# Performance work log

Measured on AMD Instinct MI355X. Metric: run time of the kernel, lower is better.

The kernel has to match this reference:

```python
import jax, jax.numpy as jnp
import numpy as np
import math

B, LQ, C = 4, 2048, 256
NH, NL, NP = 8, 4, 8
HD = C // NH
SHAPES = [(128, 128), (64, 64), (32, 32), (16, 16)]


def _grid_init_bias():
    thetas = np.arange(NH, dtype=np.float32) * (2.0 * math.pi / NH)
    g = np.stack([np.cos(thetas), np.sin(thetas)], -1)
    g = g / np.abs(g).max(-1, keepdims=True)
    g = np.tile(g[:, None, None, :], (1, NL, NP, 1))
    g = g * ((np.arange(NP, dtype=np.float32) + 1.0) / NP)[None, None, :, None]
    return jnp.asarray(g.reshape(-1), jnp.float32)


def setup_inputs() -> dict:
    key = jax.random.key(0)
    ks = jax.random.split(key, 12)
    Lv = sum(h * w for h, w in SHAPES)
    query = jax.random.normal(ks[0], (B, LQ, C), jnp.float32)
    reference_points = jax.random.uniform(ks[1], (B, LQ, NL, 2), jnp.float32)
    value = jax.random.normal(ks[2], (B, Lv, C), jnp.float32)
    spatial_shapes = jnp.asarray(np.array(SHAPES, np.int32))
    starts = np.cumsum([0] + [h * w for h, w in SHAPES])[:-1]
    level_start_index = jnp.asarray(starts.astype(np.int32))
    OFF = NH * NL * NP * 2
    return {
        'query': query,
        'reference_points': reference_points,
        'value': value,
        'spatial_shapes': spatial_shapes,
        'level_start_index': level_start_index,
        'W_off': jax.random.normal(ks[3], (C, OFF), jnp.float32) * 0.01,
        'b_off': _grid_init_bias(),
        'W_attn': jax.random.normal(ks[4], (C, NH * NL * NP), jnp.float32) * 0.01,
        'b_attn': jnp.zeros((NH * NL * NP,), jnp.float32),
        'Wa1': jax.random.normal(ks[5], (C, C // 2), jnp.float32) * 0.02,
        'ba1': jnp.zeros((C // 2,), jnp.float32),
        'Wa2': jax.random.normal(ks[6], (C // 2, OFF), jnp.float32) * 0.02,
        'ba2': jnp.zeros((OFF,), jnp.float32),
        'Wv': jax.random.normal(ks[7], (C, C), jnp.float32) * (1.0 / math.sqrt(C)),
        'bv': jnp.zeros((C,), jnp.float32),
        'Wo': jax.random.normal(ks[8], (C, C), jnp.float32) * (1.0 / math.sqrt(C)),
        'bo': jnp.zeros((C,), jnp.float32),
    }


def _bilinear(vflat, gx, gy, H, W):
    # vflat: [B, nh, H*W, hd]; gx, gy: [B, Lq, nh, P] in grid coords [-1, 1]
    # Matches F.grid_sample(mode='bilinear', padding_mode='zeros', align_corners=False)
    Bq, Lq, nh, P = gx.shape
    hd = vflat.shape[-1]
    x = ((gx + 1.0) * W - 1.0) * 0.5
    y = ((gy + 1.0) * H - 1.0) * 0.5
    x0f = jnp.floor(x); y0f = jnp.floor(y)
    lx = x - x0f; ly = y - y0f
    x0 = x0f.astype(jnp.int32); y0 = y0f.astype(jnp.int32)
    out = jnp.zeros((Bq, Lq, nh, P, hd), vflat.dtype)
    corners = ((0, 0, (1 - lx) * (1 - ly)), (1, 0, lx * (1 - ly)),
               (0, 1, (1 - lx) * ly), (1, 1, lx * ly))
    for dx, dy, w in corners:
        xi = x0 + dx; yi = y0 + dy
        valid = (xi >= 0) & (xi < W) & (yi >= 0) & (yi < H)
        idx = jnp.clip(yi, 0, H - 1) * W + jnp.clip(xi, 0, W - 1)
        idx_t = idx.transpose(0, 2, 1, 3).reshape(Bq, nh, Lq * P)
        g = jnp.take_along_axis(vflat, idx_t[..., None], axis=2)  # [B, nh, Lq*P, hd]
        g = g.reshape(Bq, nh, Lq, P, hd).transpose(0, 2, 1, 3, 4)
        out = out + g * (w * valid.astype(vflat.dtype))[..., None]
    return out


def reference(query, reference_points, value, spatial_shapes, level_start_index,
              W_off, b_off, W_attn, b_attn, Wa1, ba1, Wa2, ba2, Wv, bv, Wo, bo):
    shapes = np.asarray(spatial_shapes)
    starts = np.asarray(level_start_index)
    Bq, Lq, _ = query.shape

    v = (value @ Wv + bv).reshape(Bq, -1, NH, HD)            # [B, Lv, nh, hd]
    off = (query @ W_off + b_off).reshape(Bq, Lq, NH, NL, NP, 2)
    hid = jax.nn.relu(query @ Wa1 + ba1)
    off = off + 0.1 * (hid @ Wa2 + ba2).reshape(Bq, Lq, NH, NL, NP, 2)
    aw = jax.nn.softmax((query @ W_attn + b_attn).reshape(Bq, Lq, NH, NL * NP), -1)
    aw = aw.reshape(Bq, Lq, NH, NL, NP)

    # offset normalizer is (W, H) per level
    norm = jnp.stack([spatial_shapes[:, 1], spatial_shapes[:, 0]], -1).astype(query.dtype)
    loc = reference_points[:, :, None, :, None, :] + off / norm[None, None, None, :, None, :]
    grid = loc * 2.0 - 1.0                                    # [B, Lq, nh, NL, NP, 2]

    acc = jnp.zeros((Bq, Lq, NH, HD), query.dtype)
    for lvl in range(NL):
        H, W = int(shapes[lvl, 0]), int(shapes[lvl, 1])
        s = int(starts[lvl]); e = s + H * W
        vl = v[:, s:e].transpose(0, 2, 1, 3)                  # [B, nh, H*W, hd]
        gx = grid[:, :, :, lvl, :, 0]
        gy = grid[:, :, :, lvl, :, 1]
        samp = _bilinear(vl, gx, gy, H, W)                    # [B, Lq, nh, P, hd]
        acc = acc + jnp.einsum('blhpd,blhp->blhd', samp, aw[:, :, :, lvl, :])
    out = acc.reshape(Bq, Lq, NH * HD)
    return out @ Wo + bo
```

## Files before the change

### kernel.cpp

```cpp
#include <hip/hip_runtime.h>
#include <math.h>

#define B_SZ 4
#define LQ_SZ 2048
#define C_SZ 256
#define NH_SZ 8
#define NL_SZ 4
#define NP_SZ 8
#define HD_SZ 32
#define LV_SZ 21760
#define NQ_SZ (B_SZ * LQ_SZ)
#define MV_SZ (B_SZ * LV_SZ)

typedef __attribute__((ext_vector_type(8))) short bf16x8;
typedef __attribute__((ext_vector_type(8))) unsigned short ushort8;
typedef __attribute__((ext_vector_type(4))) float f32x4;

__device__ __forceinline__ float bf2f(unsigned short u) {
  union { float f; unsigned v; } x;
  x.v = ((unsigned)u) << 16;
  return x.f;
}
__device__ __forceinline__ unsigned short f2bf(float f) {
  union { float f; unsigned v; } x;
  x.f = f;
  unsigned r = x.v + 0x7fffu + ((x.v >> 16) & 1u);
  return (unsigned short)(r >> 16);
}

__device__ __forceinline__ bf16x8 cvt8(f32x4 a, f32x4 b) {
  union { unsigned u[4]; bf16x8 v; } r;
  asm("v_cvt_pk_bf16_f32 %0, %1, %2" : "=v"(r.u[0]) : "v"(a[0]), "v"(a[1]));
  asm("v_cvt_pk_bf16_f32 %0, %1, %2" : "=v"(r.u[1]) : "v"(a[2]), "v"(a[3]));
  asm("v_cvt_pk_bf16_f32 %0, %1, %2" : "=v"(r.u[2]) : "v"(b[0]), "v"(b[1]));
  asm("v_cvt_pk_bf16_f32 %0, %1, %2" : "=v"(r.u[3]) : "v"(b[2]), "v"(b[3]));
  return r.v;
}

__device__ __forceinline__ int swz(int x) {
  return ((x & 1) << 2) | ((x >> 1) & 3);
}

__global__ void prep_weights(
    const float* __restrict__ Wv, const float* __restrict__ Wo,
    const float* __restrict__ W_off, const float* __restrict__ W_attn,
    const float* __restrict__ Wa1, const float* __restrict__ Wa2,
    const float* __restrict__ b_off, const float* __restrict__ b_attn,
    const float* __restrict__ ba1,
    unsigned short* __restrict__ wtv, unsigned short* __restrict__ wto,
    unsigned short* __restrict__ wcat, unsigned short* __restrict__ wa2t,
    float* __restrict__ bcat) {
  const int bid = blockIdx.x, t = threadIdx.x;
  if (bid < 256) {
    wtv[bid * 256 + t] = f2bf(Wv[t * 256 + bid]);
  } else if (bid < 512) {
    const int n = bid - 256;
    wto[n * 256 + t] = f2bf(Wo[t * 256 + n]);
  } else if (bid < 1536) {
    const int n = bid - 512;
    float v;
    if (n < 512) v = W_off[t * 512 + n];
    else if (n < 768) v = W_attn[t * 256 + (n - 512)];
    else if (n < 896) v = Wa1[t * 128 + (n - 768)];
    else v = 0.f;
    wcat[n * 256 + t] = f2bf(v);
  } else if (bid < 1792) {
    const int idx = (bid - 1536) * 256 + t;
    const int n = idx >> 7, k = idx & 127;
    wa2t[n * 128 + k] = f2bf(Wa2[k * 512 + n]);
  } else {
    const int idx = (bid - 1792) * 256 + t;
    float v;
    if (idx < 512) v = b_off[idx];
    else if (idx < 768) v = b_attn[idx - 512];
    else if (idx < 896) v = ba1[idx - 768];
    else v = 0.f;
    bcat[idx] = v;
  }
}

template <int MODE, int A_BF16, int K_DIM>
__global__ __launch_bounds__(512, 2) void gemm_wave(
    const void* __restrict__ Ain, const unsigned short* __restrict__ Wt,
    const float* __restrict__ bias, void* __restrict__ Cout,
    unsigned short* __restrict__ aux, int n_total) {
  constexpr int KSTEPS = K_DIM / 32;
  constexpr int CHUNKS = K_DIM / 8;
  __shared__ unsigned short Bs[128 * K_DIM];
  const int tid = threadIdx.x;
  const int lane = tid & 63;
  const int w = tid >> 6;
  const int rowc = lane & 15, rowg = lane >> 4;
  const int bn0 = blockIdx.x * 128;
  const long bm = (long)blockIdx.y * 128;

  {
    const int row = tid >> 2, qq = tid & 3;
    const unsigned short* src = Wt + (long)(bn0 + row) * K_DIM;
    char* dstrow = (char*)Bs + row * (K_DIM * 2);
    const int sz = swz(row);
#pragma unroll
    for (int i = 0; i < CHUNKS / 4; ++i) {
      const int cl = i * 4 + qq;
      ushort8 u = *(const ushort8*)(src + cl * 8);
      *(ushort8*)(dstrow + (cl ^ sz) * 16) = u;
    }
  }

  bf16x8 afrag[KSTEPS];
  if constexpr (A_BF16) {
    const unsigned short* ap =
        (const unsigned short*)Ain + (bm + w * 16 + rowc) * (long)K_DIM +
        rowg * 8;
#pragma unroll
    for (int ks = 0; ks < KSTEPS; ++ks)
      afrag[ks] = *(const bf16x8*)(ap + ks * 32);
  } else {
    const float* ap =
        (const float*)Ain + (bm + w * 16 + rowc) * (long)K_DIM + rowg * 8;
#pragma unroll
    for (int ks = 0; ks < KSTEPS; ++ks) {
      f32x4 x0 = *(const f32x4*)(ap + ks * 32);
      f32x4 x1 = *(const f32x4*)(ap + ks * 32 + 4);
      afrag[ks] = cvt8(x0, x1);
    }
  }

  f32x4 acc[8];
#pragma unroll
  for (int n = 0; n < 8; ++n) acc[n] = (f32x4){0.f, 0.f, 0.f, 0.f};

  __syncthreads();

#pragma unroll
  for (int ks = 0; ks < KSTEPS; ++ks) {
#pragma unroll
    for (int n = 0; n < 8; ++n) {
      const int col = n * 16 + rowc;
      const int cs = (ks * 4 + rowg) ^ swz(col);
      bf16x8 bf =
          *(const bf16x8*)((const char*)Bs + col * (K_DIM * 2) + cs * 16);
      acc[n] = __builtin_amdgcn_mfma_f32_16x16x32_bf16(bf, afrag[ks], acc[n],
                                                       0, 0, 0);
    }
  }

  const long row = bm + w * 16 + rowc;
#pragma unroll
  for (int n = 0; n < 8; ++n) {
    const int col = bn0 + n * 16 + rowg * 4;
    const float4 bb = *(const float4*)(bias + col);
    const float v0 = acc[n][0] + bb.x;
    const float v1 = acc[n][1] + bb.y;
    const float v2 = acc[n][2] + bb.z;
    const float v3 = acc[n][3] + bb.w;
    if constexpr (MODE == 0) {
      float4 s = {v0, v1, v2, v3};
      *(float4*)((float*)Cout + row * n_total + col) = s;
    } else if constexpr (MODE == 1) {
      union { unsigned u[2]; uint2 d; } pk;
      asm("v_cvt_pk_bf16_f32 %0, %1, %2" : "=v"(pk.u[0]) : "v"(v0), "v"(v1));
      asm("v_cvt_pk_bf16_f32 %0, %1, %2" : "=v"(pk.u[1]) : "v"(v2), "v"(v3));
      *(uint2*)((unsigned short*)Cout + row * n_total + col) = pk.d;
    } else {
      if (bn0 < 768) {
        float4 s = {v0, v1, v2, v3};
        *(float4*)((float*)Cout + row * n_total + col) = s;
      } else {
        union { unsigned u[2]; uint2 d; } pk;
        const float r0 = fmaxf(v0, 0.f), r1 = fmaxf(v1, 0.f);
        const float r2 = fmaxf(v2, 0.f), r3 = fmaxf(v3, 0.f);
        asm("v_cvt_pk_bf16_f32 %0, %1, %2" : "=v"(pk.u[0]) : "v"(r0), "v"(r1));
        asm("v_cvt_pk_bf16_f32 %0, %1, %2" : "=v"(pk.u[1]) : "v"(r2), "v"(r3));
        *(uint2*)(aux + row * 128 + (col - 768)) = pk.d;
      }
    }
  }
}

__global__ __launch_bounds__(256) void sample_kernel(
    const unsigned short* __restrict__ v, const float* __restrict__ proj,
    const float* __restrict__ off2, const float* __restrict__ refpts,
    float* __restrict__ acc_out) {
  __shared__ int4 sidx[512];
  __shared__ float4 sw[512];
  const int tid = threadIdx.x;
  const long q0 = (long)blockIdx.x * 2;
  const int b = (int)(q0 >> 11);
  constexpr int starts[4] = {0, 16384, 20480, 21504};

#pragma unroll
  for (int ss = 0; ss < 2; ++ss) {
    const int s = tid + ss * 256;
    const int qq = s >> 8, j = s & 255;
    const long qi = q0 + qq;
    const int l = (j >> 3) & 3;
    const int HW = 128 >> l;
    const float fHW = (float)HW;

    const float logit = proj[qi * 1024 + 512 + j];
    float mx = logit;
#pragma unroll
    for (int mask = 16; mask > 0; mask >>= 1)
      mx = fmaxf(mx, __shfl_xor(mx, mask));
    const float e = __expf(logit - mx);
    float sum = e;
#pragma unroll
    for (int mask = 16; mask > 0; mask >>= 1) sum += __shfl_xor(sum, mask);
    const float wgt = e / sum;

    const float2 po = *(const float2*)(proj + qi * 1024 + 2 * j);
    const float2 o2 = *(const float2*)(off2 + qi * 512 + 2 * j);
    const float2 rp = *(const float2*)(refpts + qi * 8 + l * 2);
    const float rnorm = 1.f / fHW;
    const float gx = (rp.x + (po.x + 0.1f * o2.x) * rnorm) * 2.f - 1.f;
    const float gy = (rp.y + (po.y + 0.1f * o2.y) * rnorm) * 2.f - 1.f;

    const float x = ((gx + 1.f) * fHW - 1.f) * 0.5f;
    const float y = ((gy + 1.f) * fHW - 1.f) * 0.5f;
    const float x0f = floorf(x), y0f = floorf(y);
    const float lx = x - x0f, ly = y - y0f;
    const int ix0 = (int)x0f, iy0 = (int)y0f;
    const int ix1 = ix0 + 1, iy1 = iy0 + 1;
    const float vx0 = (ix0 >= 0 && ix0 < HW) ? 1.f : 0.f;
    const float vx1 = (ix1 >= 0 && ix1 < HW) ? 1.f : 0.f;
    const float vy0 = (iy0 >= 0 && iy0 < HW) ? 1.f : 0.f;
    const float vy1 = (iy1 >= 0 && iy1 < HW) ? 1.f : 0.f;
    const int cx0 = min(max(ix0, 0), HW - 1);
    const int cx1 = min(max(ix1, 0), HW - 1);
    const int cy0 = min(max(iy0, 0), HW - 1);
    const int cy1 = min(max(iy1, 0), HW - 1);
    const int base = starts[l];
    int4 o;
    o.x = (base + cy0 * HW + cx0) * 512;
    o.y = (base + cy0 * HW + cx1) * 512;
    o.z = (base + cy1 * HW + cx0) * 512;
    o.w = (base + cy1 * HW + cx1) * 512;
    sidx[s] = o;
    float4 wv;
    wv.x = (1.f - lx) * (1.f - ly) * vx0 * vy0 * wgt;
    wv.y = lx * (1.f - ly) * vx1 * vy0 * wgt;
    wv.z = (1.f - lx) * ly * vx0 * vy1 * wgt;
    wv.w = lx * ly * vx1 * vy1 * wgt;
    sw[s] = wv;
  }
  __syncthreads();

  const int qq = tid >> 7, h = (tid >> 4) & 7, dp = tid & 15;
  const char* vb =
      (const char*)v + ((long)b * LV_SZ * 256 + h * 32 + dp * 2) * 2;
  const int sbase = qq * 256 + h * 32;
  float acc0 = 0.f, acc1 = 0.f;
#pragma unroll 8
  for (int j = 0; j < 32; ++j) {
    const int4 o = sidx[sbase + j];
    const float4 w = sw[sbase + j];
    const ushort2 u0 = *(const ushort2*)(vb + o.x);
    const ushort2 u1 = *(const ushort2*)(vb + o.y);
    const ushort2 u2 = *(const ushort2*)(vb + o.z);
    const ushort2 u3 = *(const ushort2*)(vb + o.w);
    acc0 = fmaf(bf2f(u0.x), w.x, acc0);
    acc1 = fmaf(bf2f(u0.y), w.x, acc1);
    acc0 = fmaf(bf2f(u1.x), w.y, acc0);
    acc1 = fmaf(bf2f(u1.y), w.y, acc1);
    acc0 = fmaf(bf2f(u2.x), w.z, acc0);
    acc1 = fmaf(bf2f(u2.y), w.z, acc1);
    acc0 = fmaf(bf2f(u3.x), w.w, acc0);
    acc1 = fmaf(bf2f(u3.y), w.w, acc1);
  }
  float2 res = {acc0, acc1};
  *(float2*)(acc_out + (q0 + qq) * 256 + h * 32 + dp * 2) = res;
}

extern "C" void kernel_launch(void* const* d_in, const int* in_sizes, int n_in,
                              void* d_out, int out_size, void* d_ws,
                              size_t ws_size, hipStream_t stream) {
  const float* query  = (const float*)d_in[0];
  const float* refpts = (const float*)d_in[1];
  const float* value  = (const float*)d_in[2];
  const float* W_off  = (const float*)d_in[5];
  const float* b_off  = (const float*)d_in[6];
  const float* W_attn = (const float*)d_in[7];
  const float* b_attn = (const float*)d_in[8];
  const float* Wa1    = (const float*)d_in[9];
  const float* ba1    = (const float*)d_in[10];
  const float* Wa2    = (const float*)d_in[11];
  const float* ba2    = (const float*)d_in[12];
  const float* Wv     = (const float*)d_in[13];
  const float* bv     = (const float*)d_in[14];
  const float* Wo     = (const float*)d_in[15];
  const float* bo     = (const float*)d_in[16];
  float* out = (float*)d_out;

  char* ws = (char*)d_ws;
  unsigned short* v_ws = (unsigned short*)ws;
  float* proj_ws = (float*)(ws + 44564480);
  float* off2_ws = (float*)(ws + 78118912);
  unsigned short* wcat_ws = (unsigned short*)(ws + 78118912);
  unsigned short* hidb_ws = (unsigned short*)(ws + 94896128);
  float* acc_ws  = (float*)(ws + 96993280);
  unsigned short* wtv_ws  = (unsigned short*)(ws + 122159104);
  unsigned short* wto_ws  = (unsigned short*)(ws + 122290176);
  unsigned short* wa2t_ws = (unsigned short*)(ws + 122421248);
  float* bcat_ws = (float*)(ws + 122552320);

  prep_weights<<<1796, 256, 0, stream>>>(Wv, Wo, W_off, W_attn, Wa1, Wa2,
                                         b_off, b_attn, ba1, wtv_ws, wto_ws,
                                         wcat_ws, wa2t_ws, bcat_ws);
  gemm_wave<1, 0, 256><<<dim3(2, MV_SZ / 128), 512, 0, stream>>>(
      value, wtv_ws, bv, v_ws, nullptr, 256);
  gemm_wave<2, 0, 256><<<dim3(7, NQ_SZ / 128), 512, 0, stream>>>(
      query, wcat_ws, bcat_ws, proj_ws, hidb_ws, 1024);
  gemm_wave<0, 1, 128><<<dim3(4, NQ_SZ / 128), 512, 0, stream>>>(
      hidb_ws, wa2t_ws, ba2, off2_ws, nullptr, 512);
  sample_kernel<<<NQ_SZ / 2, 256, 0, stream>>>(v_ws, proj_ws, off2_ws, refpts,
                                               acc_ws);
  gemm_wave<0, 0, 256><<<dim3(2, NQ_SZ / 128), 512, 0, stream>>>(
      acc_ws, wto_ws, bo, out, nullptr, 256);
}
```

Before: 122.8 us.

## Make value projection GEMM persistent with weight tile reuse and A prefetch

Replaces the 1360-block value-projection GEMM with a 512-block persistent kernel. Each block loads its 128-column bf16 weight slice into LDS once and then loops over row tiles with a stride of 256. While the MFMAs for the current tile run, it prefetches and converts the next tile's fp32 A fragments in registers. This removes repeated weight staging and block launch overhead, at the cost of more registers and a possible imbalance across the 680 row tiles.

```diff
diff --git a/kernel.cpp b/kernel.cpp
--- a/kernel.cpp
+++ b/kernel.cpp
@@ -79,6 +79,93 @@
   }
 }
 
+__global__ __launch_bounds__(512, 2) void gemm_vpersist(
+    const float* __restrict__ A, const unsigned short* __restrict__ Wt,
+    const float* __restrict__ bias, unsigned short* __restrict__ Cout) {
+  __shared__ unsigned short Bs[128 * 256];
+  const int bid = blockIdx.x;
+  const int bn0 = (bid & 1) * 128;
+  const int m0 = bid >> 1;
+  const int tid = threadIdx.x;
+  const int lane = tid & 63;
+  const int w = tid >> 6;
+  const int rowc = lane & 15, rowg = lane >> 4;
+
+  {
+    const int row = tid >> 2, qq = tid & 3;
+    const unsigned short* src = Wt + (long)(bn0 + row) * 256;
+    char* dstrow = (char*)Bs + row * 512;
+    const int sz = swz(row);
+#pragma unroll
+    for (int i = 0; i < 8; ++i) {
+      const int cl = i * 4 + qq;
+      ushort8 u = *(const ushort8*)(src + cl * 8);
+      *(ushort8*)(dstrow + (cl ^ sz) * 16) = u;
+    }
+  }
+
+  const long lanoff = (long)(w * 16 + rowc) * 256 + rowg * 8;
+  bf16x8 afrag[8];
+  {
+    const float* ap = A + (long)m0 * 32768 + lanoff;
+#pragma unroll
+    for (int ks = 0; ks < 4; ++ks) {
+      f32x4 x0 = *(const f32x4*)(ap + ks * 32);
+      f32x4 x1 = *(const f32x4*)(ap + ks * 32 + 4);
+      afrag[ks] = cvt8(x0, x1);
+    }
+  }
+  __syncthreads();
+
+  for (int mt = m0; mt < 680; mt += 256) {
+    const float* apc = A + (long)mt * 32768 + lanoff;
+    const float* apn = A + (long)(mt + 256) * 32768 + lanoff;
+    const bool has_next = (mt + 256 < 680);
+
+    f32x4 acc[8];
+#pragma unroll
+    for (int n = 0; n < 8; ++n) acc[n] = (f32x4){0.f, 0.f, 0.f, 0.f};
+
+#pragma unroll
+    for (int ks = 0; ks < 8; ++ks) {
+      if constexpr (true) {
+        if (ks < 4) {
+          f32x4 x0 = *(const f32x4*)(apc + (ks + 4) * 32);
+          f32x4 x1 = *(const f32x4*)(apc + (ks + 4) * 32 + 4);
+          afrag[(ks + 4) & 7] = cvt8(x0, x1);
+        } else if (has_next) {
+          f32x4 x0 = *(const f32x4*)(apn + (ks - 4) * 32);
+          f32x4 x1 = *(const f32x4*)(apn + (ks - 4) * 32 + 4);
+          afrag[(ks - 4) & 7] = cvt8(x0, x1);
+        }
+      }
+#pragma unroll
+      for (int n = 0; n < 8; ++n) {
+        const int col = n * 16 + rowc;
+        const int cs = (ks * 4 + rowg) ^ swz(col);
+        bf16x8 bf = *(const bf16x8*)((const char*)Bs + col * 512 + cs * 16);
+        acc[n] = __builtin_amdgcn_mfma_f32_16x16x32_bf16(bf, afrag[ks],
+                                                         acc[n], 0, 0, 0);
+      }
+    }
+
+    const long row = (long)mt * 128 + w * 16 + rowc;
+#pragma unroll
+    for (int n = 0; n < 8; ++n) {
+      const int col = bn0 + n * 16 + rowg * 4;
+      const float4 bb = *(const float4*)(bias + col);
+      const float v0 = acc[n][0] + bb.x;
+      const float v1 = acc[n][1] + bb.y;
+      const float v2 = acc[n][2] + bb.z;
+      const float v3 = acc[n][3] + bb.w;
+      union { unsigned u[2]; uint2 d; } pk;
+      asm("v_cvt_pk_bf16_f32 %0, %1, %2" : "=v"(pk.u[0]) : "v"(v0), "v"(v1));
+      asm("v_cvt_pk_bf16_f32 %0, %1, %2" : "=v"(pk.u[1]) : "v"(v2), "v"(v3));
+      *(uint2*)(Cout + row * 256 + col) = pk.d;
+    }
+  }
+}
+
 template <int MODE, int A_BF16, int K_DIM>
 __global__ __launch_bounds__(512, 2) void gemm_wave(
     const void* __restrict__ Ain, const unsigned short* __restrict__ Wt,
@@ -307,8 +394,7 @@
   prep_weights<<<1796, 256, 0, stream>>>(Wv, Wo, W_off, W_attn, Wa1, Wa2,
                                          b_off, b_attn, ba1, wtv_ws, wto_ws,
                                          wcat_ws, wa2t_ws, bcat_ws);
-  gemm_wave<1, 0, 256><<<dim3(2, MV_SZ / 128), 512, 0, stream>>>(
-      value, wtv_ws, bv, v_ws, nullptr, 256);
+  gemm_vpersist<<<512, 512, 0, stream>>>(value, wtv_ws, bv, v_ws);
   gemm_wave<2, 0, 256><<<dim3(7, NQ_SZ / 128), 512, 0, stream>>>(
       query, wcat_ws, bcat_ws, proj_ws, hidb_ws, 1024);
   gemm_wave<0, 1, 128><<<dim3(4, NQ_SZ / 128), 512, 0, stream>>>(
```

After: 122.5 us. About the same (-0.2%).
